# Kernel tuning notes

Measured on AMD Instinct MI355X. Metric: run time of the kernel, lower is better.

Reference implementation:

```python
import jax, jax.numpy as jnp
import numpy as np

NHEAD = 8
NPTS = 4

def _bilinear_sample(E_flat, locs, H, W):
    # E_flat: [B, H*W, D] channel-last flattened feature map
    # locs:   [B, N, 2] normalized (x, y) in [-1, 1], align_corners=False, zeros padding
    ix = ((locs[..., 0] + 1.0) * W - 1.0) * 0.5
    iy = ((locs[..., 1] + 1.0) * H - 1.0) * 0.5
    x0 = jnp.floor(ix); y0 = jnp.floor(iy)
    x1 = x0 + 1.0;      y1 = y0 + 1.0
    wx1 = ix - x0; wx0 = 1.0 - wx1
    wy1 = iy - y0; wy0 = 1.0 - wy1
    gather = jax.vmap(lambda e, i: e[i])  # per-batch gather -> [B, N, D]
    def corner(xc, yc, w):
        valid = (xc >= 0) & (xc < W) & (yc >= 0) & (yc < H)
        xi = jnp.clip(xc, 0, W - 1).astype(jnp.int32)
        yi = jnp.clip(yc, 0, H - 1).astype(jnp.int32)
        g = gather(E_flat, yi * W + xi)
        return g * (w * valid)[..., None]
    return (corner(x0, y0, wx0 * wy0) + corner(x1, y0, wx1 * wy0)
            + corner(x0, y1, wx0 * wy1) + corner(x1, y1, wx1 * wy1))

def setup_inputs() -> dict:
    key = jax.random.key(0)
    ks = jax.random.split(key, 6)
    B, M, D = 8, 1024, 256
    H, Wd = 100, 100
    SADQ = jax.random.normal(ks[0], (B, M, D), jnp.float32)
    E = jax.random.normal(ks[1], (B, H * Wd, D), jnp.float32)
    # learned params (random instead of the degenerate zero-init, so the math is exercised)
    Wo = jax.random.normal(ks[2], (D, NHEAD * NPTS * 2), jnp.float32) * 0.02
    bo = jnp.zeros((NHEAD * NPTS * 2,), jnp.float32)
    Wa = jax.random.normal(ks[3], (D, NHEAD * NPTS), jnp.float32) * 0.05
    ba = jnp.zeros((NHEAD * NPTS,), jnp.float32)
    Wr = jax.random.normal(ks[4], (D, 2), jnp.float32) * 0.05
    br = jnp.zeros((2,), jnp.float32)
    Wp = jax.random.normal(ks[5], (D, D), jnp.float32) * 0.05
    bp = jnp.zeros((D,), jnp.float32)
    return {"SADQ": SADQ, "E": E, "Wo": Wo, "bo": bo, "Wa": Wa, "ba": ba,
            "Wr": Wr, "br": br, "Wp": Wp, "bp": bp, "H": H, "W": Wd}

def reference(SADQ, E, Wo, bo, Wa, ba, Wr, br, Wp, bp, H, W):
    B, M, D = SADQ.shape
    offsets = (SADQ @ Wo + bo).reshape(B, M, NHEAD, NPTS, 2)
    attn = jax.nn.softmax((SADQ @ Wa + ba).reshape(B, M, NHEAD, NPTS), axis=-1)
    base_ref = (SADQ @ Wr + br)[:, :, None, None, :]            # [B, M, 1, 1, 2]
    locs = (base_ref + offsets * 0.1).reshape(B, M * NHEAD * NPTS, 2)
    sampled = _bilinear_sample(E, locs, H, W).reshape(B, M, NHEAD, NPTS, D)
    # sum over points, mean over heads, fused into one contraction
    agg = jnp.einsum('bmhpd,bmhp->bmd', sampled, attn) / NHEAD
    return agg @ Wp + bp
```

## Files before the change

kernel.cpp:

```cpp
#include <hip/hip_runtime.h>
#include <hip/hip_bf16.h>
#include <math.h>

#define BATCH 8
#define MQ    1024
#define DIM   256
#define NHEAD 8
#define NPTS  4
#define NPROJ 98
#define NCORN (NHEAD * NPTS * 4)

typedef __attribute__((ext_vector_type(8))) short  short8;
typedef __attribute__((ext_vector_type(4))) float  f32x4;

static __device__ __forceinline__ ushort f2bf(float f) {
    union { float f; unsigned u; } v; v.f = f;
    const unsigned r = v.u + 0x7fffu + ((v.u >> 16) & 1u);
    return (ushort)(r >> 16);
}

__global__ __launch_bounds__(256) void fused_sample_kernel(
    const float* __restrict__ SADQ,
    const float* __restrict__ E,
    const float* __restrict__ Wo, const float* __restrict__ bo,
    const float* __restrict__ Wa, const float* __restrict__ ba,
    const float* __restrict__ Wr, const float* __restrict__ br,
    const int*   __restrict__ Hp, const int* __restrict__ Wdp,
    ushort* __restrict__ aggb)
{
    const int row = blockIdx.x;
    const int b   = row / MQ;
    const int tid = threadIdx.x;

    __shared__ float  qs[DIM];
    __shared__ float  proj[128];
    __shared__ float  partial[128];
    __shared__ float  sW[NCORN];
    __shared__ int    sIdx[NCORN];
    __shared__ float4 red[4][64];

    qs[tid] = SADQ[(size_t)row * DIM + tid];
    __syncthreads();

    {
        const int j    = tid & 127;
        const int half = tid >> 7;
        float s = 0.f, bias = 0.f;
        if (j < NPROJ) {
            const float* Wb; int col, ncols;
            if (j < 64)      { Wb = Wo; col = j;      ncols = 64; bias = bo[col]; }
            else if (j < 96) { Wb = Wa; col = j - 64; ncols = 32; bias = ba[col]; }
            else             { Wb = Wr; col = j - 96; ncols = 2;  bias = br[col]; }
            const float* wp = Wb + (size_t)(half * 128) * ncols + col;
            const float* qp = qs + half * 128;
            #pragma unroll 8
            for (int d = 0; d < 128; ++d)
                s = fmaf(qp[d], wp[(size_t)d * ncols], s);
        }
        if (half) partial[j] = s;
        __syncthreads();
        if (!half && j < NPROJ) proj[j] = s + bias + partial[j];
        __syncthreads();
    }

    const int Hh = *Hp;
    const int Ww = *Wdp;
    if (tid < NHEAD * NPTS) {
        const int p = tid;
        const int h = p >> 2;
        const float l0 = proj[64 + h * 4 + 0];
        const float l1 = proj[64 + h * 4 + 1];
        const float l2 = proj[64 + h * 4 + 2];
        const float l3 = proj[64 + h * 4 + 3];
        const float mx = fmaxf(fmaxf(l0, l1), fmaxf(l2, l3));
        const float e0 = expf(l0 - mx), e1 = expf(l1 - mx),
                    e2 = expf(l2 - mx), e3 = expf(l3 - mx);
        const float inv = 1.f / (e0 + e1 + e2 + e3);
        const float aw  = expf(proj[64 + p] - mx) * inv * (1.f / NHEAD);

        const float lx = proj[96] + 0.1f * proj[p * 2 + 0];
        const float ly = proj[97] + 0.1f * proj[p * 2 + 1];
        const float ix = ((lx + 1.f) * (float)Ww - 1.f) * 0.5f;
        const float iy = ((ly + 1.f) * (float)Hh - 1.f) * 0.5f;
        const float x0f = floorf(ix), y0f = floorf(iy);
        const int   x0  = (int)x0f,   y0  = (int)y0f;
        const float wx1 = ix - x0f, wx0 = 1.f - wx1;
        const float wy1 = iy - y0f, wy0 = 1.f - wy1;

        #pragma unroll
        for (int c = 0; c < 4; ++c) {
            const int   xc = x0 + (c & 1);
            const int   yc = y0 + (c >> 1);
            const float wx = (c & 1) ? wx1 : wx0;
            const float wy = (c >> 1) ? wy1 : wy0;
            const bool valid = (xc >= 0) && (xc < Ww) && (yc >= 0) && (yc < Hh);
            const int xi = min(max(xc, 0), Ww - 1);
            const int yi = min(max(yc, 0), Hh - 1);
            sW  [p * 4 + c] = valid ? (wx * wy * aw) : 0.f;
            sIdx[p * 4 + c] = (yi * Ww + xi) * (DIM / 4);
        }
    }
    __syncthreads();

    const int cg  = tid >> 6;
    const int ch4 = tid & 63;
    const float4* __restrict__ Eb4 =
        (const float4*)(E + (size_t)b * (size_t)(Hh * Ww) * DIM);

    float4 acc = make_float4(0.f, 0.f, 0.f, 0.f);
    #pragma unroll
    for (int t = 0; t < 32; ++t) {
        const int   i   = cg * 32 + t;
        const float w   = sW[i];
        const int   idx = sIdx[i];
        const float4 e  = Eb4[(size_t)idx + ch4];
        acc.x = fmaf(w, e.x, acc.x);
        acc.y = fmaf(w, e.y, acc.y);
        acc.z = fmaf(w, e.z, acc.z);
        acc.w = fmaf(w, e.w, acc.w);
    }
    red[cg][ch4] = acc;
    __syncthreads();

    if (cg == 0) {
        const float4 r0 = red[0][ch4];
        const float4 r1 = red[1][ch4];
        const float4 r2 = red[2][ch4];
        const float4 r3 = red[3][ch4];
        ushort4 o;
        o.x = f2bf((r0.x + r1.x) + (r2.x + r3.x));
        o.y = f2bf((r0.y + r1.y) + (r2.y + r3.y));
        o.z = f2bf((r0.z + r1.z) + (r2.z + r3.z));
        o.w = f2bf((r0.w + r1.w) + (r2.w + r3.w));
        *(ushort4*)&aggb[(size_t)row * DIM + ch4 * 4] = o;
    }
}

__global__ __launch_bounds__(256) void wp_convert_kernel(
    const float* __restrict__ Wp, ushort* __restrict__ WpT)
{
    const int k = blockIdx.x;
    const int n = threadIdx.x;
    WpT[(size_t)n * DIM + k] = f2bf(Wp[(size_t)k * DIM + n]);
}

__global__ __launch_bounds__(256) void mfma_gemm_kernel(
    const ushort* __restrict__ A,
    const ushort* __restrict__ BT,
    const float*  __restrict__ bp,
    float* __restrict__ out)
{
    __shared__ ushort ldsA[64 * 40];
    __shared__ ushort ldsB[64 * 40];

    const int tid  = threadIdx.x;
    const int mb   = blockIdx.x * 64;
    const int nb   = blockIdx.y * 64;
    const int wave = tid >> 6;
    const int lane = tid & 63;
    const int r0   = (wave >> 1) * 32;
    const int c0   = (wave & 1) * 32;
    const int lrow = lane & 15;
    const int kgrp = lane >> 4;

    const int sm = tid >> 2;
    const int sc = (tid & 3) * 8;

    f32x4 acc00 = {0.f, 0.f, 0.f, 0.f};
    f32x4 acc01 = {0.f, 0.f, 0.f, 0.f};
    f32x4 acc10 = {0.f, 0.f, 0.f, 0.f};
    f32x4 acc11 = {0.f, 0.f, 0.f, 0.f};

    for (int kb = 0; kb < DIM; kb += 32) {
        *(uint4*)&ldsA[sm * 40 + sc] =
            *(const uint4*)&A[(size_t)(mb + sm) * DIM + kb + sc];
        *(uint4*)&ldsB[sm * 40 + sc] =
            *(const uint4*)&BT[(size_t)(nb + sm) * DIM + kb + sc];
        __syncthreads();

        const short8 a0 = *(const short8*)&ldsA[(r0 + lrow)      * 40 + kgrp * 8];
        const short8 a1 = *(const short8*)&ldsA[(r0 + 16 + lrow) * 40 + kgrp * 8];
        const short8 b0 = *(const short8*)&ldsB[(c0 + lrow)      * 40 + kgrp * 8];
        const short8 b1 = *(const short8*)&ldsB[(c0 + 16 + lrow) * 40 + kgrp * 8];

        acc00 = __builtin_amdgcn_mfma_f32_16x16x32_bf16(a0, b0, acc00, 0, 0, 0);
        acc01 = __builtin_amdgcn_mfma_f32_16x16x32_bf16(a0, b1, acc01, 0, 0, 0);
        acc10 = __builtin_amdgcn_mfma_f32_16x16x32_bf16(a1, b0, acc10, 0, 0, 0);
        acc11 = __builtin_amdgcn_mfma_f32_16x16x32_bf16(a1, b1, acc11, 0, 0, 0);
        __syncthreads();
    }

    const int orow = mb + r0 + kgrp * 4;
    const int ocol = nb + c0 + lrow;
    const float bp0 = bp[ocol];
    const float bp1 = bp[ocol + 16];
    #pragma unroll
    for (int reg = 0; reg < 4; ++reg) {
        out[(size_t)(orow + reg)      * DIM + ocol]      = acc00[reg] + bp0;
        out[(size_t)(orow + reg)      * DIM + ocol + 16] = acc01[reg] + bp1;
        out[(size_t)(orow + 16 + reg) * DIM + ocol]      = acc10[reg] + bp0;
        out[(size_t)(orow + 16 + reg) * DIM + ocol + 16] = acc11[reg] + bp1;
    }
}

extern "C" void kernel_launch(void* const* d_in, const int* in_sizes, int n_in,
                              void* d_out, int out_size, void* d_ws, size_t ws_size,
                              hipStream_t stream)
{
    const float* SADQ = (const float*)d_in[0];
    const float* E    = (const float*)d_in[1];
    const float* Wo   = (const float*)d_in[2];
    const float* bo   = (const float*)d_in[3];
    const float* Wa   = (const float*)d_in[4];
    const float* ba   = (const float*)d_in[5];
    const float* Wr   = (const float*)d_in[6];
    const float* br   = (const float*)d_in[7];
    const float* Wp   = (const float*)d_in[8];
    const float* bp   = (const float*)d_in[9];
    const int*   Hp   = (const int*)d_in[10];
    const int*   Wdp  = (const int*)d_in[11];

    const int BM = in_sizes[0] / DIM;

    ushort* aggb = (ushort*)d_ws;
    ushort* WpT  = (ushort*)((char*)d_ws + (size_t)BM * DIM * 2);
    float*  out  = (float*)d_out;

    fused_sample_kernel<<<BM, 256, 0, stream>>>(
        SADQ, E, Wo, bo, Wa, ba, Wr, br, Hp, Wdp, aggb);

    wp_convert_kernel<<<DIM, 256, 0, stream>>>(Wp, WpT);

    dim3 g2(BM / 64, DIM / 64);
    mfma_gemm_kernel<<<g2, 256, 0, stream>>>(aggb, WpT, bp, out);
}
```

Measured before the change: 216.2 us.

## Deduplicate bilinear corner pixels per query via shared-memory grid before gathering

Before gathering feature rows, each query block computes the bounding box of its valid corner pixels. If the box fits in a 32x32 window, weights for identical pixels are merged in a shared-memory grid with atomics and compacted into a shorter list, so each distinct E row is fetched once. Otherwise it falls back to the original 128-corner loop. This trades extra atomics, a 1024-cell grid scan and more barriers for fewer global gathers. Results change only slightly through reordered float accumulation.

```diff
diff --git a/kernel.cpp b/kernel.cpp
--- a/kernel.cpp
+++ b/kernel.cpp
@@ -1,6 +1,7 @@
 #include <hip/hip_runtime.h>
 #include <hip/hip_bf16.h>
 #include <math.h>
+#include <limits.h>
 
 #define BATCH 8
 #define MQ    1024
@@ -9,6 +10,7 @@
 #define NPTS  4
 #define NPROJ 98
 #define NCORN (NHEAD * NPTS * 4)
+#define GRIDW 32
 
 typedef __attribute__((ext_vector_type(8))) short  short8;
 typedef __attribute__((ext_vector_type(4))) float  f32x4;
@@ -38,8 +40,20 @@
     __shared__ float  sW[NCORN];
     __shared__ int    sIdx[NCORN];
     __shared__ float4 red[4][64];
+    __shared__ float  grid[GRIDW * GRIDW];
+    __shared__ float  sWd[NCORN];
+    __shared__ int    sIdxd[NCORN];
+    __shared__ int    sBBox[4];
+    __shared__ int    sCnt;
 
     qs[tid] = SADQ[(size_t)row * DIM + tid];
+    if (tid == 0) {
+        sBBox[0] = INT_MAX; sBBox[1] = INT_MAX;
+        sBBox[2] = INT_MIN; sBBox[3] = INT_MIN;
+        sCnt = 0;
+    }
+    #pragma unroll
+    for (int c = tid; c < GRIDW * GRIDW; c += 256) grid[c] = 0.f;
     __syncthreads();
 
     {
@@ -102,22 +116,75 @@
     }
     __syncthreads();
 
+    if (tid < NCORN) {
+        const float w = sW[tid];
+        if (w > 0.f) {
+            const int pix = sIdx[tid] >> 6;
+            const int x = pix % Ww;
+            const int y = pix / Ww;
+            atomicMin(&sBBox[0], x); atomicMin(&sBBox[1], y);
+            atomicMax(&sBBox[2], x); atomicMax(&sBBox[3], y);
+        }
+    }
+    __syncthreads();
+
+    const int xmin = sBBox[0], ymin = sBBox[1];
+    const bool fits = (xmin != INT_MAX) &&
+                      (sBBox[2] - xmin < GRIDW) && (sBBox[3] - ymin < GRIDW);
+
+    if (fits) {
+        if (tid < NCORN) {
+            const float w = sW[tid];
+            if (w > 0.f) {
+                const int pix = sIdx[tid] >> 6;
+                const int x = pix % Ww;
+                const int y = pix / Ww;
+                atomicAdd(&grid[(y - ymin) * GRIDW + (x - xmin)], w);
+            }
+        }
+        __syncthreads();
+        for (int c = tid; c < GRIDW * GRIDW; c += 256) {
+            const float w = grid[c];
+            if (w != 0.f) {
+                const int pos = atomicAdd(&sCnt, 1);
+                const int x = xmin + (c & (GRIDW - 1));
+                const int y = ymin + (c >> 5);
+                sWd[pos]   = w;
+                sIdxd[pos] = (y * Ww + x) * (DIM / 4);
+            }
+        }
+        __syncthreads();
+    }
+
     const int cg  = tid >> 6;
     const int ch4 = tid & 63;
     const float4* __restrict__ Eb4 =
         (const float4*)(E + (size_t)b * (size_t)(Hh * Ww) * DIM);
 
     float4 acc = make_float4(0.f, 0.f, 0.f, 0.f);
-    #pragma unroll
-    for (int t = 0; t < 32; ++t) {
-        const int   i   = cg * 32 + t;
-        const float w   = sW[i];
-        const int   idx = sIdx[i];
-        const float4 e  = Eb4[(size_t)idx + ch4];
-        acc.x = fmaf(w, e.x, acc.x);
-        acc.y = fmaf(w, e.y, acc.y);
-        acc.z = fmaf(w, e.z, acc.z);
-        acc.w = fmaf(w, e.w, acc.w);
+    if (fits) {
+        const int n = sCnt;
+        for (int i = cg; i < n; i += 4) {
+            const float w   = sWd[i];
+            const int   idx = sIdxd[i];
+            const float4 e  = Eb4[(size_t)idx + ch4];
+            acc.x = fmaf(w, e.x, acc.x);
+            acc.y = fmaf(w, e.y, acc.y);
+            acc.z = fmaf(w, e.z, acc.z);
+            acc.w = fmaf(w, e.w, acc.w);
+        }
+    } else {
+        #pragma unroll 8
+        for (int t = 0; t < 32; ++t) {
+            const int   i   = cg * 32 + t;
+            const float w   = sW[i];
+            const int   idx = sIdx[i];
+            const float4 e  = Eb4[(size_t)idx + ch4];
+            acc.x = fmaf(w, e.x, acc.x);
+            acc.y = fmaf(w, e.y, acc.y);
+            acc.z = fmaf(w, e.z, acc.z);
+            acc.w = fmaf(w, e.w, acc.w);
+        }
     }
     red[cg][ch4] = acc;
     __syncthreads();
```

Result: slower. 227.5 us (+5.2%).

## Split projection into tiled GEMM kernel and gather with one wave per query

Applied to the files above, without the earlier changes.

The per-row projection, previously a naive dot product in each sampling block reading strided weights, moves to its own kernel. That kernel packs Wo/Wa/Wr into one padded weight matrix and runs a shared-memory tiled GEMM over 32 query rows per block. The gather kernel now gives each query a single wave that walks all 128 corners, with 8 loads in flight per iteration, so the LDS cross-group reduction is gone. The cost is two extra launches and a round trip of the projection through global memory.

```diff
diff --git a/kernel.cpp b/kernel.cpp
--- a/kernel.cpp
+++ b/kernel.cpp
@@ -8,7 +8,7 @@
 #define NHEAD 8
 #define NPTS  4
 #define NPROJ 98
-#define NCORN (NHEAD * NPTS * 4)
+#define PSTR  112
 
 typedef __attribute__((ext_vector_type(8))) short  short8;
 typedef __attribute__((ext_vector_type(4))) float  f32x4;
@@ -19,67 +19,112 @@
     return (ushort)(r >> 16);
 }
 
-__global__ __launch_bounds__(256) void fused_sample_kernel(
-    const float* __restrict__ SADQ,
-    const float* __restrict__ E,
+#define KEEP4(v) asm volatile("" : "+v"(v.x), "+v"(v.y), "+v"(v.z), "+v"(v.w))
+
+__global__ __launch_bounds__(112) void wcat_build_kernel(
     const float* __restrict__ Wo, const float* __restrict__ bo,
     const float* __restrict__ Wa, const float* __restrict__ ba,
     const float* __restrict__ Wr, const float* __restrict__ br,
+    float* __restrict__ Wcat, float* __restrict__ bcat)
+{
+    const int k = blockIdx.x;
+    const int j = threadIdx.x;
+    float w = 0.f, bias = 0.f;
+    if (j < 64)      { w = Wo[k * 64 + j];        bias = bo[j]; }
+    else if (j < 96) { w = Wa[k * 32 + (j - 64)]; bias = ba[j - 64]; }
+    else if (j < 98) { w = Wr[k * 2  + (j - 96)]; bias = br[j - 96]; }
+    Wcat[k * PSTR + j] = w;
+    if (k == 0) bcat[j] = bias;
+}
+
+__global__ __launch_bounds__(256) void proj_kernel(
+    const float* __restrict__ SADQ,
+    const float* __restrict__ Wcat,
+    const float* __restrict__ bcat,
+    float* __restrict__ P)
+{
+    __shared__ float Qs[32][65];
+    __shared__ float Ws[64][112];
+
+    const int tid  = threadIdx.x;
+    const int row0 = blockIdx.x * 32;
+    const int rg   = tid >> 4;
+    const int cg   = tid & 15;
+
+    float acc0[7] = {};
+    float acc1[7] = {};
+
+    for (int kc = 0; kc < DIM; kc += 64) {
+        #pragma unroll
+        for (int i = 0; i < 2; ++i) {
+            const int fi = tid * 2 + i;
+            const int r  = fi >> 4;
+            const int k4 = (fi & 15) * 4;
+            const float4 v = *(const float4*)&SADQ[(size_t)(row0 + r) * DIM + kc + k4];
+            Qs[r][k4 + 0] = v.x; Qs[r][k4 + 1] = v.y;
+            Qs[r][k4 + 2] = v.z; Qs[r][k4 + 3] = v.w;
+        }
+        for (int fi = tid; fi < 64 * 28; fi += 256) {
+            const int k  = fi / 28;
+            const int j4 = (fi % 28) * 4;
+            *(float4*)&Ws[k][j4] = *(const float4*)&Wcat[(size_t)(kc + k) * PSTR + j4];
+        }
+        __syncthreads();
+
+        #pragma unroll 8
+        for (int k = 0; k < 64; ++k) {
+            const float q0 = Qs[rg * 2 + 0][k];
+            const float q1 = Qs[rg * 2 + 1][k];
+            #pragma unroll
+            for (int j = 0; j < 7; ++j) {
+                const float w = Ws[k][cg * 7 + j];
+                acc0[j] = fmaf(q0, w, acc0[j]);
+                acc1[j] = fmaf(q1, w, acc1[j]);
+            }
+        }
+        __syncthreads();
+    }
+
+    #pragma unroll
+    for (int j = 0; j < 7; ++j) {
+        const int col = cg * 7 + j;
+        const float bb = bcat[col];
+        P[(size_t)(row0 + rg * 2 + 0) * PSTR + col] = acc0[j] + bb;
+        P[(size_t)(row0 + rg * 2 + 1) * PSTR + col] = acc1[j] + bb;
+    }
+}
+
+__global__ __launch_bounds__(256) void gather_kernel(
+    const float* __restrict__ P,
+    const float* __restrict__ E,
     const int*   __restrict__ Hp, const int* __restrict__ Wdp,
     ushort* __restrict__ aggb)
 {
-    const int row = blockIdx.x;
-    const int b   = row / MQ;
-    const int tid = threadIdx.x;
-
-    __shared__ float  qs[DIM];
-    __shared__ float  proj[128];
-    __shared__ float  partial[128];
-    __shared__ float  sW[NCORN];
-    __shared__ int    sIdx[NCORN];
-    __shared__ float4 red[4][64];
-
-    qs[tid] = SADQ[(size_t)row * DIM + tid];
-    __syncthreads();
-
-    {
-        const int j    = tid & 127;
-        const int half = tid >> 7;
-        float s = 0.f, bias = 0.f;
-        if (j < NPROJ) {
-            const float* Wb; int col, ncols;
-            if (j < 64)      { Wb = Wo; col = j;      ncols = 64; bias = bo[col]; }
-            else if (j < 96) { Wb = Wa; col = j - 64; ncols = 32; bias = ba[col]; }
-            else             { Wb = Wr; col = j - 96; ncols = 2;  bias = br[col]; }
-            const float* wp = Wb + (size_t)(half * 128) * ncols + col;
-            const float* qp = qs + half * 128;
-            #pragma unroll 8
-            for (int d = 0; d < 128; ++d)
-                s = fmaf(qp[d], wp[(size_t)d * ncols], s);
-        }
-        if (half) partial[j] = s;
-        __syncthreads();
-        if (!half && j < NPROJ) proj[j] = s + bias + partial[j];
-        __syncthreads();
-    }
+    const int tid  = threadIdx.x;
+    const int wid  = tid >> 6;
+    const int lane = tid & 63;
+    const int row  = blockIdx.x * 4 + wid;
+    const int b    = row >> 10;
+
+    __shared__ float sW[4][128];
+    __shared__ int   sIdx[4][128];
 
     const int Hh = *Hp;
     const int Ww = *Wdp;
-    if (tid < NHEAD * NPTS) {
-        const int p = tid;
-        const int h = p >> 2;
-        const float l0 = proj[64 + h * 4 + 0];
-        const float l1 = proj[64 + h * 4 + 1];
-        const float l2 = proj[64 + h * 4 + 2];
-        const float l3 = proj[64 + h * 4 + 3];
-        const float mx = fmaxf(fmaxf(l0, l1), fmaxf(l2, l3));
-        const float e0 = expf(l0 - mx), e1 = expf(l1 - mx),
-                    e2 = expf(l2 - mx), e3 = expf(l3 - mx);
-        const float inv = 1.f / (e0 + e1 + e2 + e3);
-        const float aw  = expf(proj[64 + p] - mx) * inv * (1.f / NHEAD);
-
-        const float lx = proj[96] + 0.1f * proj[p * 2 + 0];
-        const float ly = proj[97] + 0.1f * proj[p * 2 + 1];
+
+    if (lane < 32) {
+        const int p = lane;
+        const float* Pr = P + (size_t)row * PSTR;
+        const float lg = Pr[64 + p];
+        float mx = fmaxf(lg, __shfl_xor(lg, 1));
+        mx = fmaxf(mx, __shfl_xor(mx, 2));
+        const float e = expf(lg - mx);
+        float s = e + __shfl_xor(e, 1);
+        s += __shfl_xor(s, 2);
+        const float aw = e / s * (1.f / NHEAD);
+
+        const float lx = Pr[96] + 0.1f * Pr[p * 2 + 0];
+        const float ly = Pr[97] + 0.1f * Pr[p * 2 + 1];
         const float ix = ((lx + 1.f) * (float)Ww - 1.f) * 0.5f;
         const float iy = ((ly + 1.f) * (float)Hh - 1.f) * 0.5f;
         const float x0f = floorf(ix), y0f = floorf(iy);
@@ -96,44 +141,59 @@
             const bool valid = (xc >= 0) && (xc < Ww) && (yc >= 0) && (yc < Hh);
             const int xi = min(max(xc, 0), Ww - 1);
             const int yi = min(max(yc, 0), Hh - 1);
-            sW  [p * 4 + c] = valid ? (wx * wy * aw) : 0.f;
-            sIdx[p * 4 + c] = (yi * Ww + xi) * (DIM / 4);
+            sW  [wid][p * 4 + c] = valid ? (wx * wy * aw) : 0.f;
+            sIdx[wid][p * 4 + c] = (yi * Ww + xi) * (DIM / 4);
         }
     }
     __syncthreads();
 
-    const int cg  = tid >> 6;
-    const int ch4 = tid & 63;
     const float4* __restrict__ Eb4 =
         (const float4*)(E + (size_t)b * (size_t)(Hh * Ww) * DIM);
 
     float4 acc = make_float4(0.f, 0.f, 0.f, 0.f);
-    #pragma unroll
-    for (int t = 0; t < 32; ++t) {
-        const int   i   = cg * 32 + t;
-        const float w   = sW[i];
-        const int   idx = sIdx[i];
-        const float4 e  = Eb4[(size_t)idx + ch4];
-        acc.x = fmaf(w, e.x, acc.x);
-        acc.y = fmaf(w, e.y, acc.y);
-        acc.z = fmaf(w, e.z, acc.z);
-        acc.w = fmaf(w, e.w, acc.w);
-    }
-    red[cg][ch4] = acc;
-    __syncthreads();
-
-    if (cg == 0) {
-        const float4 r0 = red[0][ch4];
-        const float4 r1 = red[1][ch4];
-        const float4 r2 = red[2][ch4];
-        const float4 r3 = red[3][ch4];
-        ushort4 o;
-        o.x = f2bf((r0.x + r1.x) + (r2.x + r3.x));
-        o.y = f2bf((r0.y + r1.y) + (r2.y + r3.y));
-        o.z = f2bf((r0.z + r1.z) + (r2.z + r3.z));
-        o.w = f2bf((r0.w + r1.w) + (r2.w + r3.w));
-        *(ushort4*)&aggb[(size_t)row * DIM + ch4 * 4] = o;
-    }
+    for (int t = 0; t < 128; t += 8) {
+        const float w0 = sW[wid][t + 0]; const int i0 = sIdx[wid][t + 0];
+        const float w1 = sW[wid][t + 1]; const int i1 = sIdx[wid][t + 1];
+        const float w2 = sW[wid][t + 2]; const int i2 = sIdx[wid][t + 2];
+        const float w3 = sW[wid][t + 3]; const int i3 = sIdx[wid][t + 3];
+        const float w4 = sW[wid][t + 4]; const int i4 = sIdx[wid][t + 4];
+        const float w5 = sW[wid][t + 5]; const int i5 = sIdx[wid][t + 5];
+        const float w6 = sW[wid][t + 6]; const int i6 = sIdx[wid][t + 6];
+        const float w7 = sW[wid][t + 7]; const int i7 = sIdx[wid][t + 7];
+
+        float4 e0 = Eb4[(size_t)i0 + lane];
+        float4 e1 = Eb4[(size_t)i1 + lane];
+        float4 e2 = Eb4[(size_t)i2 + lane];
+        float4 e3 = Eb4[(size_t)i3 + lane];
+        float4 e4 = Eb4[(size_t)i4 + lane];
+        float4 e5 = Eb4[(size_t)i5 + lane];
+        float4 e6 = Eb4[(size_t)i6 + lane];
+        float4 e7 = Eb4[(size_t)i7 + lane];
+        KEEP4(e0); KEEP4(e1); KEEP4(e2); KEEP4(e3);
+        KEEP4(e4); KEEP4(e5); KEEP4(e6); KEEP4(e7);
+
+        acc.x = fmaf(w0, e0.x, acc.x); acc.y = fmaf(w0, e0.y, acc.y);
+        acc.z = fmaf(w0, e0.z, acc.z); acc.w = fmaf(w0, e0.w, acc.w);
+        acc.x = fmaf(w1, e1.x, acc.x); acc.y = fmaf(w1, e1.y, acc.y);
+        acc.z = fmaf(w1, e1.z, acc.z); acc.w = fmaf(w1, e1.w, acc.w);
+        acc.x = fmaf(w2, e2.x, acc.x); acc.y = fmaf(w2, e2.y, acc.y);
+        acc.z = fmaf(w2, e2.z, acc.z); acc.w = fmaf(w2, e2.w, acc.w);
+        acc.x = fmaf(w3, e3.x, acc.x); acc.y = fmaf(w3, e3.y, acc.y);
+        acc.z = fmaf(w3, e3.z, acc.z); acc.w = fmaf(w3, e3.w, acc.w);
+        acc.x = fmaf(w4, e4.x, acc.x); acc.y = fmaf(w4, e4.y, acc.y);
+        acc.z = fmaf(w4, e4.z, acc.z); acc.w = fmaf(w4, e4.w, acc.w);
+        acc.x = fmaf(w5, e5.x, acc.x); acc.y = fmaf(w5, e5.y, acc.y);
+        acc.z = fmaf(w5, e5.z, acc.z); acc.w = fmaf(w5, e5.w, acc.w);
+        acc.x = fmaf(w6, e6.x, acc.x); acc.y = fmaf(w6, e6.y, acc.y);
+        acc.z = fmaf(w6, e6.z, acc.z); acc.w = fmaf(w6, e6.w, acc.w);
+        acc.x = fmaf(w7, e7.x, acc.x); acc.y = fmaf(w7, e7.y, acc.y);
+        acc.z = fmaf(w7, e7.z, acc.z); acc.w = fmaf(w7, e7.w, acc.w);
+    }
+
+    ushort4 o;
+    o.x = f2bf(acc.x); o.y = f2bf(acc.y);
+    o.z = f2bf(acc.z); o.w = f2bf(acc.w);
+    *(ushort4*)&aggb[(size_t)row * DIM + lane * 4] = o;
 }
 
 __global__ __launch_bounds__(256) void wp_convert_kernel(
@@ -222,13 +282,17 @@
 
     const int BM = in_sizes[0] / DIM;
 
-    ushort* aggb = (ushort*)d_ws;
-    ushort* WpT  = (ushort*)((char*)d_ws + (size_t)BM * DIM * 2);
+    char* ws = (char*)d_ws;
+    ushort* aggb = (ushort*)(ws);
+    ushort* WpT  = (ushort*)(ws + 4194304);
+    float*  P    = (float*) (ws + 4194304 + 131072);
+    float*  Wcat = (float*) (ws + 4194304 + 131072 + 3670016);
+    float*  bcat = (float*) (ws + 4194304 + 131072 + 3670016 + 114688);
     float*  out  = (float*)d_out;
 
-    fused_sample_kernel<<<BM, 256, 0, stream>>>(
-        SADQ, E, Wo, bo, Wa, ba, Wr, br, Hp, Wdp, aggb);
-
+    wcat_build_kernel<<<DIM, PSTR, 0, stream>>>(Wo, bo, Wa, ba, Wr, br, Wcat, bcat);
+    proj_kernel<<<BM / 32, 256, 0, stream>>>(SADQ, Wcat, bcat, P);
+    gather_kernel<<<BM / 4, 256, 0, stream>>>(P, E, Hp, Wdp, aggb);
     wp_convert_kernel<<<DIM, 256, 0, stream>>>(Wp, WpT);
 
     dim3 g2(BM / 64, DIM / 64);
```

New measurement: 217.3 us. No clear change (+0.5%).
